# Performance work log

Hardware: AMD Instinct MI355X
Metric: run time of the kernel (lower is better)

Reference implementation:

```python
import jax, jax.numpy as jnp
import numpy as np

NUM, NUM_TOP, COBJ = 32, 32, 4   # num = MBS*ncobj, num_top, cobj_size = k//2
B, D, H = 300, 256, 256          # bag_size, feature dim, relation hidden
K_OBJ = 8                        # k (output cobj size)
FEA0 = 2 * NUM * COBJ            # orig_fea leading dim = MBS*K with K=2*ncobj*cobj_size


def setup_inputs() -> dict:
    key = jax.random.key(0)
    ks = jax.random.split(key, 8)
    return {
        "orig_fea": jax.random.normal(ks[0], (FEA0, B, D), dtype=jnp.float32),
        "ind0": jax.random.randint(ks[1], (NUM, NUM_TOP, COBJ), 0, B, dtype=jnp.int32),
        "ind1": jax.random.randint(ks[2], (NUM, NUM_TOP, COBJ), 0, B, dtype=jnp.int32),
        "k": K_OBJ,
        "W1a": jax.random.normal(ks[3], (D, H), dtype=jnp.float32) * (1.0 / np.sqrt(D)),
        "W1b": jax.random.normal(ks[4], (D, H), dtype=jnp.float32) * (1.0 / np.sqrt(D)),
        "b1": jnp.zeros((H,), dtype=jnp.float32),
        "W2": jax.random.normal(ks[5], (H, 1), dtype=jnp.float32) * (1.0 / np.sqrt(H)),
        "b2": jnp.zeros((1,), dtype=jnp.float32),
    }


def reference(orig_fea, ind0, ind1, k, W1a, W1b, b1, W2, b2):
    num, num_top, cobj = ind0.shape
    bag = orig_fea.shape[1]
    d = orig_fea.shape[2]
    # create_ids: stride bag_size over cobj positions -> [num, L], L = num_top*cobj
    off = (bag * jnp.arange(cobj, dtype=ind0.dtype))
    ids0 = (ind0 + off).reshape(num, -1)
    ids1 = (ind1 + off).reshape(num, -1)
    # rsolo_fea = reshape(orig_fea, [num, 2, pool, D]); pool = cobj*bag
    pool = (orig_fea.shape[0] * bag) // (2 * num)
    rsolo = orig_fea.reshape(num, 2, pool, d)
    # gather per-side features (dedup+inverse-gather in the original is an
    # optimization; direct gather yields the identical score matrix)
    f0 = jnp.take_along_axis(rsolo[:, 0], ids0[..., None], axis=1)  # [num, L, D]
    f1 = jnp.take_along_axis(rsolo[:, 1], ids1[..., None], axis=1)  # [num, L, D]
    # relation unit: score(a,b) = MLP(concat(f0_a, f1_b)) -> [num, L, L, 1]
    h0 = jnp.einsum('nad,dh->nah', f0, W1a)          # [num, L, H]
    h1 = jnp.einsum('nbd,dh->nbh', f1, W1b)          # [num, L, H]
    h = jax.nn.relu(h0[:, :, None, :] + h1[:, None, :, :] + b1)  # [num, L, L, H]
    scores = jnp.einsum('nabh,ho->nabo', h, W2) + b2              # [num, L, L, 1]
    # sum_kxk_patches with patch size k//2
    kp = k // 2
    L = num_top * cobj
    hk = L // kp
    scores = scores.reshape(num, hk, kp, hk, kp, 1).sum(axis=(2, 4))  # [num, m, l, 1]
    m = l = num_top
    scores = scores.reshape(num, m * l, 1)
    # get_pairs
    pairs = jnp.stack(jnp.meshgrid(jnp.arange(m, dtype=jnp.int32),
                                   jnp.arange(l, dtype=jnp.int32), indexing='ij'),
                      axis=-1).reshape(1, m * l, 2)
    pairs = jnp.broadcast_to(pairs, (num, m * l, 2))
    return scores, pairs
```

## Files before the change

kernel.cpp:

```cpp
#include <hip/hip_runtime.h>

#define NUMB 32
#define LL   128
#define POOL 1200
#define BAG  300
#define DD   256
#define HH   256
#define NS   (NUMB*32*32)

using bf16x8 = __bf16    __attribute__((ext_vector_type(8)));
using f32x4  = float     __attribute__((ext_vector_type(4)));
using fp16x2 = __fp16    __attribute__((ext_vector_type(2)));
using h16x2  = _Float16  __attribute__((ext_vector_type(2)));
using h16x8  = _Float16  __attribute__((ext_vector_type(8)));

typedef const __attribute__((address_space(1))) unsigned int* gas_t;
typedef       __attribute__((address_space(3))) unsigned int* las_t;

static __device__ __forceinline__ unsigned short f2bf(float x) {
    unsigned u = __float_as_uint(x);
    return (unsigned short)((u + 0x7FFFu + ((u >> 16) & 1u)) >> 16);
}

static __device__ __forceinline__ float pkh(float a, float b) {
    fp16x2 p = __builtin_amdgcn_cvt_pkrtz(a, b);
    return __builtin_bit_cast(float, p);
}

__global__ __launch_bounds__(256) void k_prep(
    const float* __restrict__ W1a, const float* __restrict__ W1b,
    unsigned short* __restrict__ WtP, float* __restrict__ out)
{
    const int blk = blockIdx.x, t = threadIdx.x;
    if (blk < 32) {
        const int side = blk >> 4, kc = blk & 15;
        const float* W = side ? W1b : W1a;
        __shared__ float T[16][257];
        const int row = t >> 4, c = t & 15;
#pragma unroll
        for (int i = 0; i < 4; ++i) {
            int col4 = c + i * 16;
            float4 v = *(const float4*)(W + (size_t)(kc * 16 + row) * HH + col4 * 4);
            T[row][col4 * 4 + 0] = v.x; T[row][col4 * 4 + 1] = v.y;
            T[row][col4 * 4 + 2] = v.z; T[row][col4 * 4 + 3] = v.w;
        }
        __syncthreads();
        const int n = t, ht = n >> 6, nn = n & 63;
#pragma unroll
        for (int j = 0; j < 2; ++j) {
            unsigned short tmp[8] __attribute__((aligned(16)));
#pragma unroll
            for (int e = 0; e < 8; ++e) tmp[e] = f2bf(T[j * 8 + e][n]);
            int U = kc * 2 + j;
            int pos = U ^ (nn & 7);
            size_t unit = ((size_t)((side * 4 + ht) * 64 + nn)) * 32 + pos;
            *(float4*)(WtP + unit * 8) = *(float4*)tmp;
        }
    } else {
        int G = (blk - 32) * 256 + t;
        int local = G & 511;
        float i = (float)(local >> 4);
        float c0 = (float)((2 * local) & 31);
        ((float4*)(out + NS))[G] = make_float4(i, c0, i, c0 + 1.0f);
    }
}

__global__ __launch_bounds__(256) void k_gemm(
    const float* __restrict__ fea,
    const int*   __restrict__ ind0,
    const int*   __restrict__ ind1,
    const float* __restrict__ b1,
    const unsigned short* __restrict__ WtP,
    unsigned short* __restrict__ Hh)
{
    __shared__ unsigned short As[64 * 256] __attribute__((aligned(16)));
    __shared__ unsigned short Bs[64 * 256] __attribute__((aligned(16)));

    int b = blockIdx.x;
    const int ht = b & 3, rt = b >> 2;
    const int side = rt >> 6;
    const int R0 = rt * 64;
    const int t = threadIdx.x, w = t >> 6, lane = t & 63;

    const unsigned short* Wbase = WtP + ((size_t)(side * 4 + ht)) * 64 * 256;
#pragma unroll
    for (int i = 0; i < 8; ++i) {
        int chunk = w * 8 + i;
        __builtin_amdgcn_global_load_lds(
            (gas_t)(const void*)(Wbase + chunk * 512 + lane * 8),
            (las_t)(void*)(As + chunk * 512),
            16, 0, 0);
    }

    {
        const int lr = t >> 2;
        const int g = R0 + lr;
        const int rs = g & 4095, n_ = rs >> 7, a_ = rs & 127;
        const int id = (side ? ind1 : ind0)[n_ * LL + a_] + BAG * (a_ & 3);
        const float* arow = fea + (size_t)((n_ * 2 + side) * POOL + id) * DD;
        const int sw = lr & 7;
#pragma unroll
        for (int j0 = 0; j0 < 16; ++j0) {
            int jj = j0 * 4 + (t & 3);
            float4 v = *(const float4*)(arow + jj * 4);
            unsigned short tmp[4] __attribute__((aligned(8)));
            tmp[0] = f2bf(v.x); tmp[1] = f2bf(v.y);
            tmp[2] = f2bf(v.z); tmp[3] = f2bf(v.w);
            int u = jj >> 1, pos = u ^ sw;
            *(double*)&Bs[lr * 256 + pos * 8 + (jj & 1) * 4] = *(double*)tmp;
        }
    }
    __syncthreads();

    const int l15 = lane & 15, q = lane >> 4;
    f32x4 acc[4] = {};
#pragma unroll
    for (int kk = 0; kk < 8; ++kk) {
        const int u = kk * 4 + q;
        const int hr = w * 16 + l15;
        bf16x8 af = *(const bf16x8*)&As[hr * 256 + (u ^ (hr & 7)) * 8];
        bf16x8 bf[4];
#pragma unroll
        for (int rb = 0; rb < 4; ++rb) {
            int r = rb * 16 + l15;
            bf[rb] = *(const bf16x8*)&Bs[r * 256 + (u ^ (r & 7)) * 8];
        }
#pragma unroll
        for (int rb = 0; rb < 4; ++rb)
            acc[rb] = __builtin_amdgcn_mfma_f32_16x16x32_bf16(af, bf[rb], acc[rb], 0, 0, 0);
    }

    const int hbase = ht * 64 + w * 16 + q * 4;
    float4 bias = make_float4(0.f, 0.f, 0.f, 0.f);
    if (side == 0) bias = *(const float4*)(b1 + hbase);
#pragma unroll
    for (int rb = 0; rb < 4; ++rb) {
        int frow = R0 + rb * 16 + l15;
        float2 pk;
        pk.x = pkh(acc[rb][0] + bias.x, acc[rb][1] + bias.y);
        pk.y = pkh(acc[rb][2] + bias.z, acc[rb][3] + bias.w);
        *(float2*)&Hh[(size_t)frow * HH + hbase] = pk;
    }
}

__global__ __launch_bounds__(256) void k_pair(
    const unsigned short* __restrict__ Hh,
    const float* __restrict__ W2,
    const float* __restrict__ b2,
    float*       __restrict__ out)
{
    __shared__ unsigned short s0[32 * 256] __attribute__((aligned(16)));
    __shared__ unsigned short s1[32 * 256] __attribute__((aligned(16)));
    __shared__ unsigned short w2s[256]     __attribute__((aligned(16)));
    __shared__ float sred[256];

    int b = blockIdx.x;
    const int jt = b & 3;  b >>= 2;
    const int it = b & 3;  b >>= 2;
    const int n  = b;
    const int t = threadIdx.x, w = t >> 6, lane = t & 63;

    const size_t base0 = ((size_t)(n * LL) + it * 32) * HH;
    const size_t base1 = ((size_t)(NUMB * LL + n * LL) + jt * 32) * HH;

    {
        const int pos = lane & 31, rhalf = lane >> 5;
#pragma unroll
        for (int i = 0; i < 4; ++i) {
            int rowbase = w * 8 + i * 2;
            int row = rowbase + rhalf;
            int f = pos ^ ((row >> 2) & 7);
            __builtin_amdgcn_global_load_lds(
                (gas_t)(const void*)(Hh + base0 + (size_t)row * HH + f * 8),
                (las_t)(void*)(s0 + rowbase * 256), 16, 0, 0);
            __builtin_amdgcn_global_load_lds(
                (gas_t)(const void*)(Hh + base1 + (size_t)row * HH + f * 8),
                (las_t)(void*)(s1 + rowbase * 256), 16, 0, 0);
        }
    }
    if (t < 64) {
        float4 v = *(const float4*)(W2 + t * 4);
        float2 pk;
        pk.x = pkh(v.x, v.y);
        pk.y = pkh(v.z, v.w);
        *(float2*)&w2s[t * 4] = pk;
    }
    __syncthreads();

    const int il = (t >> 3) & 7, jl = t & 7;
    float acc[4][4] = {{0.f,0.f,0.f,0.f},{0.f,0.f,0.f,0.f},
                       {0.f,0.f,0.f,0.f},{0.f,0.f,0.f,0.f}};

#pragma unroll
    for (int f = 0; f < 8; ++f) {
        h16x8 wv = *(const h16x8*)&w2s[(w * 8 + f) * 8];
        const h16x2* wp = (const h16x2*)&wv;
        h16x8 av[4], bv[4];
#pragma unroll
        for (int r = 0; r < 4; ++r)
            av[r] = *(const h16x8*)&s0[(il * 4 + r) * 256 + (w * 8 + (f ^ il)) * 8];
#pragma unroll
        for (int s = 0; s < 4; ++s)
            bv[s] = *(const h16x8*)&s1[(jl * 4 + s) * 256 + (w * 8 + (f ^ jl)) * 8];
        const h16x8 zero = {0, 0, 0, 0, 0, 0, 0, 0};
#pragma unroll
        for (int r = 0; r < 4; ++r)
#pragma unroll
            for (int s = 0; s < 4; ++s) {
                h16x8 sum = av[r] + bv[s];
                sum = __builtin_elementwise_max(sum, zero);
                const h16x2* sp = (const h16x2*)&sum;
#pragma unroll
                for (int u = 0; u < 4; ++u)
                    acc[r][s] = __builtin_amdgcn_fdot2(sp[u], wp[u], acc[r][s], false);
            }
    }

    float total = 0.f;
#pragma unroll
    for (int r = 0; r < 4; ++r)
#pragma unroll
        for (int s = 0; s < 4; ++s) total += acc[r][s];

    sred[t] = total;
    __syncthreads();

    if (t < 64) {
        float sum = sred[t] + sred[t + 64] + sred[t + 128] + sred[t + 192]
                  + 16.0f * b2[0];
        int i = it * 8 + (t >> 3);
        int j = jt * 8 + (t & 7);
        out[n * 1024 + i * 32 + j] = sum;
    }
}

extern "C" void kernel_launch(void* const* d_in, const int* in_sizes, int n_in,
                              void* d_out, int out_size, void* d_ws, size_t ws_size,
                              hipStream_t stream)
{
    const float* fea  = (const float*)d_in[0];
    const int*   ind0 = (const int*)  d_in[1];
    const int*   ind1 = (const int*)  d_in[2];
    const float* W1a  = (const float*)d_in[4];
    const float* W1b  = (const float*)d_in[5];
    const float* b1   = (const float*)d_in[6];
    const float* W2   = (const float*)d_in[7];
    const float* b2   = (const float*)d_in[8];
    float* out = (float*)d_out;

    unsigned short* WtP = (unsigned short*)d_ws;
    unsigned short* Hh  = (unsigned short*)((char*)d_ws + 512 * 1024);

    hipLaunchKernelGGL(k_prep, dim3(96), dim3(256), 0, stream,
                       W1a, W1b, WtP, out);
    hipLaunchKernelGGL(k_gemm, dim3(512), dim3(256), 0, stream,
                       fea, ind0, ind1, b1, WtP, Hh);
    hipLaunchKernelGGL(k_pair, dim3(512), dim3(256), 0, stream,
                       Hh, W2, b2, out);
}
```

Before: 132.6 us.

## Retile GEMM warps 2x2, pack bf16 in hardware, remap blocks across XCDs

The GEMM kernel now splits its 64x64 tile across warps as a 2x2 grid of 32x32 subtiles instead of 16 rows per warp. This lowers the LDS fragment reads per MFMA. Feature conversion uses the v_cvt_pk_bf16_f32 instruction with 16-byte LDS stores in place of software rounding. Both kernels remap block indices so neighbouring tiles land on the same XCD. Writing the pair indices moves from the prep kernel into the pair kernel's epilogue, which shrinks the prep launch.

```diff
diff --git a/kernel.cpp b/kernel.cpp
--- a/kernel.cpp
+++ b/kernel.cpp
@@ -27,41 +27,39 @@
     return __builtin_bit_cast(float, p);
 }
 
+static __device__ __forceinline__ unsigned int pkbf(float a, float b) {
+    unsigned int r;
+    asm("v_cvt_pk_bf16_f32 %0, %1, %2" : "=v"(r) : "v"(a), "v"(b));
+    return r;
+}
+
 __global__ __launch_bounds__(256) void k_prep(
     const float* __restrict__ W1a, const float* __restrict__ W1b,
-    unsigned short* __restrict__ WtP, float* __restrict__ out)
+    unsigned short* __restrict__ WtP)
 {
     const int blk = blockIdx.x, t = threadIdx.x;
-    if (blk < 32) {
-        const int side = blk >> 4, kc = blk & 15;
-        const float* W = side ? W1b : W1a;
-        __shared__ float T[16][257];
-        const int row = t >> 4, c = t & 15;
-#pragma unroll
-        for (int i = 0; i < 4; ++i) {
-            int col4 = c + i * 16;
-            float4 v = *(const float4*)(W + (size_t)(kc * 16 + row) * HH + col4 * 4);
-            T[row][col4 * 4 + 0] = v.x; T[row][col4 * 4 + 1] = v.y;
-            T[row][col4 * 4 + 2] = v.z; T[row][col4 * 4 + 3] = v.w;
-        }
-        __syncthreads();
-        const int n = t, ht = n >> 6, nn = n & 63;
-#pragma unroll
-        for (int j = 0; j < 2; ++j) {
-            unsigned short tmp[8] __attribute__((aligned(16)));
-#pragma unroll
-            for (int e = 0; e < 8; ++e) tmp[e] = f2bf(T[j * 8 + e][n]);
-            int U = kc * 2 + j;
-            int pos = U ^ (nn & 7);
-            size_t unit = ((size_t)((side * 4 + ht) * 64 + nn)) * 32 + pos;
-            *(float4*)(WtP + unit * 8) = *(float4*)tmp;
-        }
-    } else {
-        int G = (blk - 32) * 256 + t;
-        int local = G & 511;
-        float i = (float)(local >> 4);
-        float c0 = (float)((2 * local) & 31);
-        ((float4*)(out + NS))[G] = make_float4(i, c0, i, c0 + 1.0f);
+    const int side = blk >> 4, kc = blk & 15;
+    const float* W = side ? W1b : W1a;
+    __shared__ float T[16][257];
+    const int row = t >> 4, c = t & 15;
+#pragma unroll
+    for (int i = 0; i < 4; ++i) {
+        int col4 = c + i * 16;
+        float4 v = *(const float4*)(W + (size_t)(kc * 16 + row) * HH + col4 * 4);
+        T[row][col4 * 4 + 0] = v.x; T[row][col4 * 4 + 1] = v.y;
+        T[row][col4 * 4 + 2] = v.z; T[row][col4 * 4 + 3] = v.w;
+    }
+    __syncthreads();
+    const int n = t, ht = n >> 6, nn = n & 63;
+#pragma unroll
+    for (int j = 0; j < 2; ++j) {
+        unsigned short tmp[8] __attribute__((aligned(16)));
+#pragma unroll
+        for (int e = 0; e < 8; ++e) tmp[e] = f2bf(T[j * 8 + e][n]);
+        int U = kc * 2 + j;
+        int pos = U ^ (nn & 7);
+        size_t unit = ((size_t)((side * 4 + ht) * 64 + nn)) * 32 + pos;
+        *(float4*)(WtP + unit * 8) = *(float4*)tmp;
     }
 }
 
@@ -76,7 +74,8 @@
     __shared__ unsigned short As[64 * 256] __attribute__((aligned(16)));
     __shared__ unsigned short Bs[64 * 256] __attribute__((aligned(16)));
 
-    int b = blockIdx.x;
+    const int b0 = blockIdx.x;
+    const int b = (b0 & 7) * 64 + (b0 >> 3);
     const int ht = b & 3, rt = b >> 2;
     const int side = rt >> 6;
     const int R0 = rt * 64;
@@ -100,46 +99,62 @@
         const float* arow = fea + (size_t)((n_ * 2 + side) * POOL + id) * DD;
         const int sw = lr & 7;
 #pragma unroll
-        for (int j0 = 0; j0 < 16; ++j0) {
-            int jj = j0 * 4 + (t & 3);
-            float4 v = *(const float4*)(arow + jj * 4);
-            unsigned short tmp[4] __attribute__((aligned(8)));
-            tmp[0] = f2bf(v.x); tmp[1] = f2bf(v.y);
-            tmp[2] = f2bf(v.z); tmp[3] = f2bf(v.w);
-            int u = jj >> 1, pos = u ^ sw;
-            *(double*)&Bs[lr * 256 + pos * 8 + (jj & 1) * 4] = *(double*)tmp;
+        for (int j0 = 0; j0 < 8; ++j0) {
+            int u = j0 * 4 + (t & 3);
+            float4 v0 = *(const float4*)(arow + u * 8);
+            float4 v1 = *(const float4*)(arow + u * 8 + 4);
+            unsigned int tmp[4] __attribute__((aligned(16)));
+            tmp[0] = pkbf(v0.x, v0.y);
+            tmp[1] = pkbf(v0.z, v0.w);
+            tmp[2] = pkbf(v1.x, v1.y);
+            tmp[3] = pkbf(v1.z, v1.w);
+            int pos = u ^ sw;
+            *(f32x4*)&Bs[lr * 256 + pos * 8] = *(const f32x4*)tmp;
         }
     }
     __syncthreads();
 
     const int l15 = lane & 15, q = lane >> 4;
-    f32x4 acc[4] = {};
+    const int wh = w >> 1, wr = w & 1;
+    f32x4 acc[2][2] = {};
 #pragma unroll
     for (int kk = 0; kk < 8; ++kk) {
         const int u = kk * 4 + q;
-        const int hr = w * 16 + l15;
-        bf16x8 af = *(const bf16x8*)&As[hr * 256 + (u ^ (hr & 7)) * 8];
-        bf16x8 bf[4];
-#pragma unroll
-        for (int rb = 0; rb < 4; ++rb) {
-            int r = rb * 16 + l15;
-            bf[rb] = *(const bf16x8*)&Bs[r * 256 + (u ^ (r & 7)) * 8];
-        }
-#pragma unroll
-        for (int rb = 0; rb < 4; ++rb)
-            acc[rb] = __builtin_amdgcn_mfma_f32_16x16x32_bf16(af, bf[rb], acc[rb], 0, 0, 0);
-    }
-
-    const int hbase = ht * 64 + w * 16 + q * 4;
-    float4 bias = make_float4(0.f, 0.f, 0.f, 0.f);
-    if (side == 0) bias = *(const float4*)(b1 + hbase);
-#pragma unroll
-    for (int rb = 0; rb < 4; ++rb) {
-        int frow = R0 + rb * 16 + l15;
+        bf16x8 af[2], bfv[2];
+#pragma unroll
+        for (int a = 0; a < 2; ++a) {
+            int hr = wh * 32 + a * 16 + l15;
+            af[a] = *(const bf16x8*)&As[hr * 256 + (u ^ (hr & 7)) * 8];
+        }
+#pragma unroll
+        for (int r = 0; r < 2; ++r) {
+            int rr = wr * 32 + r * 16 + l15;
+            bfv[r] = *(const bf16x8*)&Bs[rr * 256 + (u ^ (rr & 7)) * 8];
+        }
+#pragma unroll
+        for (int a = 0; a < 2; ++a)
+#pragma unroll
+            for (int r = 0; r < 2; ++r)
+                acc[a][r] = __builtin_amdgcn_mfma_f32_16x16x32_bf16(af[a], bfv[r], acc[a][r], 0, 0, 0);
+    }
+
+    const int hq = ht * 64 + wh * 32 + q * 4;
+    float4 bias[2];
+    bias[0] = make_float4(0.f, 0.f, 0.f, 0.f);
+    bias[1] = bias[0];
+    if (side == 0) {
+        bias[0] = *(const float4*)(b1 + hq);
+        bias[1] = *(const float4*)(b1 + hq + 16);
+    }
+#pragma unroll
+    for (int a = 0; a < 2; ++a)
+#pragma unroll
+    for (int r = 0; r < 2; ++r) {
+        int frow = R0 + wr * 32 + r * 16 + l15;
         float2 pk;
-        pk.x = pkh(acc[rb][0] + bias.x, acc[rb][1] + bias.y);
-        pk.y = pkh(acc[rb][2] + bias.z, acc[rb][3] + bias.w);
-        *(float2*)&Hh[(size_t)frow * HH + hbase] = pk;
+        pk.x = pkh(acc[a][r][0] + bias[a].x, acc[a][r][1] + bias[a].y);
+        pk.y = pkh(acc[a][r][2] + bias[a].z, acc[a][r][3] + bias[a].w);
+        *(float2*)&Hh[(size_t)frow * HH + hq + a * 16] = pk;
     }
 }
 
@@ -154,7 +169,8 @@
     __shared__ unsigned short w2s[256]     __attribute__((aligned(16)));
     __shared__ float sred[256];
 
-    int b = blockIdx.x;
+    const int b0 = blockIdx.x;
+    int b = (b0 & 7) * 64 + (b0 >> 3);
     const int jt = b & 3;  b >>= 2;
     const int it = b & 3;  b >>= 2;
     const int n  = b;
@@ -230,7 +246,9 @@
                   + 16.0f * b2[0];
         int i = it * 8 + (t >> 3);
         int j = jt * 8 + (t & 7);
-        out[n * 1024 + i * 32 + j] = sum;
+        int p = n * 1024 + i * 32 + j;
+        out[p] = sum;
+        *(float2*)(out + NS + 2 * p) = make_float2((float)i, (float)j);
     }
 }
 
@@ -251,8 +269,8 @@
     unsigned short* WtP = (unsigned short*)d_ws;
     unsigned short* Hh  = (unsigned short*)((char*)d_ws + 512 * 1024);
 
-    hipLaunchKernelGGL(k_prep, dim3(96), dim3(256), 0, stream,
-                       W1a, W1b, WtP, out);
+    hipLaunchKernelGGL(k_prep, dim3(32), dim3(256), 0, stream,
+                       W1a, W1b, WtP);
     hipLaunchKernelGGL(k_gemm, dim3(512), dim3(256), 0, stream,
                        fea, ind0, ind1, b1, WtP, Hh);
     hipLaunchKernelGGL(k_pair, dim3(512), dim3(256), 0, stream,
```

Measured after the change: 129.6 us. -2.3%, faster.
